# Kernel optimization log

Measured on AMD Instinct MI355X. Metric: run time of the kernel, lower is better.

Reference implementation:

```python
import jax, jax.numpy as jnp
import numpy as np


def setup_inputs() -> dict:
    key = jax.random.key(0)
    k1, k2, k3 = jax.random.split(key, 3)
    N, Ci, H, W = 16, 64, 224, 224
    Co, K = 128, 3
    x = jax.random.normal(k1, (N, Ci, H, W), dtype=jnp.float32)
    # Kaiming-like scale for conv weight
    conv_weight = jax.random.normal(k2, (Co, Ci, K, K), dtype=jnp.float32) * (1.0 / np.sqrt(Ci * K * K))
    conv_bias = jax.random.normal(k3, (Co,), dtype=jnp.float32) * 0.01
    return {"x": x, "conv_weight": conv_weight, "conv_bias": conv_bias}


def reference(x, conv_weight, conv_bias):
    # conv2d, stride=1, padding=0 (VALID), NCHW / OIHW
    y = jax.lax.conv_general_dilated(
        x, conv_weight,
        window_strides=(1, 1),
        padding="VALID",
        dimension_numbers=("NCHW", "OIHW", "NCHW"),
    ) + conv_bias[None, :, None, None]  # [N, Co, OH, OW]
    # min over output channels (keepdim), then double tanh
    m = jnp.min(y, axis=1, keepdims=True)  # [N, 1, OH, OW]
    return jnp.tanh(jnp.tanh(m))
```

## Files before the change

### kernel.cpp

```cpp
#include <hip/hip_runtime.h>
#include <hip/hip_bf16.h>
#include <math.h>

#define NN   16
#define CI   64
#define HH   224
#define WW   224
#define CO   128
#define OHH  222
#define OWW  222

#define WS_NEED (36*4*64*16)

typedef short  short8  __attribute__((ext_vector_type(8)));
typedef float  f32x16  __attribute__((ext_vector_type(16)));
typedef float  f32x4   __attribute__((ext_vector_type(4)));

__device__ static inline unsigned f2bf_pk(float a, float b) {
  __hip_bfloat162 h = __float22bfloat162_rn(make_float2(a, b));
  return *reinterpret_cast<unsigned*>(&h);
}

__global__ __launch_bounds__(256) void prep_w_kernel(const float* __restrict__ wt,
                                                     unsigned char* __restrict__ ws) {
  int t    = blockIdx.x * 256 + threadIdx.x;
  int lane = t & 63;
  int f    = t >> 6;
  int s    = f >> 2;
  int ct   = f & 3;
  int tap  = s >> 2;
  int cic  = s & 3;
  int kh   = tap / 3, kw = tap % 3;
  int co   = ct * 32 + (lane & 31);
  int k0   = cic * 16 + (lane >> 5) * 8;
  unsigned pk[4];
#pragma unroll
  for (int j = 0; j < 4; ++j) {
    int ci0 = k0 + 2 * j;
    float a = wt[(size_t)co * 576 + (ci0    ) * 9 + kh * 3 + kw];
    float b = wt[(size_t)co * 576 + (ci0 + 1) * 9 + kh * 3 + kw];
    pk[j] = f2bf_pk(a, b);
  }
  ((uint4*)ws)[t] = make_uint4(pk[0], pk[1], pk[2], pk[3]);
}

__global__ __launch_bounds__(512, 4) void conv_min_kernel(
    const float* __restrict__ x, const float* __restrict__ bias,
    const unsigned char* __restrict__ ws, float* __restrict__ out) {
  __shared__ __align__(16) unsigned char smem[6 * 34 * 128];

  int bid = blockIdx.x;
  bid = (bid & 7) * (NN * 56 * 7 / 8) + (bid >> 3);

  int owt  = bid % 7;
  int rest = bid / 7;
  int oht  = rest % 56;
  int n    = rest / 56;
  int ow0  = (owt < 6) ? owt * 32 : 190;
  int oh0  = oht * 4;

  int tid   = threadIdx.x;
  int wv    = tid >> 6;
  int lane  = tid & 63;
  int mg    = wv >> 1;
  int ng    = wv & 1;
  int mrow  = lane & 31;
  int khalf = lane >> 5;

  const short8* wf = (const short8*)ws;
  int bbase = ng * 128 + lane;
  short8 bb[3][2];
#pragma unroll
  for (int ct = 0; ct < 2; ++ct) bb[0][ct] = wf[0 * 256 + ct * 64 + bbase];
#pragma unroll
  for (int ct = 0; ct < 2; ++ct) bb[1][ct] = wf[1 * 256 + ct * 64 + bbase];

  {
    const float* xb = x + (size_t)n * 64 * 50176;
    int colm = (tid & 15) * 2;
    int q    = tid >> 4;
    int cc   = q >> 2, jw = (q & 3) * 4;
    int w0off = (((cc + colm    ) & 7) << 4) + jw;
    int w1off = (((cc + colm + 1) & 7) << 4) + jw;
    const float* xm = xb + (size_t)(q * 2) * 50176 + ow0 + colm;
    float2 A2[6], B2[6];
#pragma unroll
    for (int r = 0; r < 6; ++r) {
      int rg = oh0 + r; if (rg > 223) rg = 223;
      const float* s0 = xm + (size_t)rg * 224;
      A2[r] = *(const float2*)s0;
      B2[r] = *(const float2*)(s0 + 50176);
    }
    int re   = tid >> 6;
    int cole = 32 + ((tid >> 5) & 1);
    int ppe  = tid & 31;
    float ea = 0.f, eb = 0.f;
    const float* xe = xb + (size_t)(ppe * 2) * 50176 + ow0 + cole;
    if (re < 6) {
      int rg = oh0 + re; if (rg > 223) rg = 223;
      ea = xe[(size_t)rg * 224];
      eb = xe[(size_t)rg * 224 + 50176];
    }
#pragma unroll
    for (int r = 0; r < 6; ++r) {
      unsigned u0 = f2bf_pk(A2[r].x, B2[r].x);
      unsigned u1 = f2bf_pk(A2[r].y, B2[r].y);
      *(unsigned*)(smem + (r * 34 + colm    ) * 128 + w0off) = u0;
      *(unsigned*)(smem + (r * 34 + colm + 1) * 128 + w1off) = u1;
    }
    if (re < 6) {
      int eoff = ((((ppe >> 2) + cole) & 7) << 4) + (ppe & 3) * 4;
      *(unsigned*)(smem + (re * 34 + cole) * 128 + eoff) = f2bf_pk(ea, eb);
    }
  }

  f32x16 acc[2];
#pragma unroll
  for (int ct = 0; ct < 2; ++ct) {
    float bv = bias[ng * 64 + ct * 32 + mrow];
#pragma unroll
    for (int r = 0; r < 16; ++r) acc[ct][r] = bv;
  }

  unsigned uu = (mrow + khalf) & 7;
  const unsigned char* Pb = smem + (mg * 34 + mrow) * 128;
  const unsigned char* P[8];
#pragma unroll
  for (int j = 0; j < 8; ++j) P[j] = Pb + ((uu + j) & 7) * 16;

  __syncthreads();

  short8 aa[3];
  aa[0] = *(const short8*)(P[0]);
  aa[1] = *(const short8*)(P[2]);

#pragma unroll
  for (int s = 0; s < 36; ++s) {
    if (s + 2 < 36) {
#pragma unroll
      for (int ct = 0; ct < 2; ++ct)
        bb[(s + 2) % 3][ct] = wf[(s + 2) * 256 + ct * 64 + bbase];
      const int s2 = s + 2;
      const int kh2 = s2 / 12, kw2 = (s2 / 4) % 3, cic2 = s2 & 3;
      const int j2 = (2 * cic2 + kw2) & 7;
      aa[s2 % 3] = *(const short8*)(P[j2] + ((kh2 * 34 + kw2) << 7));
    }
#pragma unroll
    for (int ct = 0; ct < 2; ++ct)
      acc[ct] = __builtin_amdgcn_mfma_f32_32x32x16_bf16(
          aa[s % 3], bb[s % 3][ct], acc[ct], 0, 0, 0);
  }

  __syncthreads();
  float* epi = (float*)smem;
#pragma unroll
  for (int r = 0; r < 16; ++r) {
    float v = fminf(acc[0][r], acc[1][r]);
    v = fminf(v, __shfl_xor(v, 16, 64));
    if ((lane & 16) == 0) {
      int px = mg * 32 + ((r & 3) + 8 * (r >> 2) + 4 * khalf);
      epi[px * 36 + ng * 16 + (lane & 15)] = v;
    }
  }
  __syncthreads();
  if (tid < 128) {
    int px = tid;
    int oh = oh0 + (px >> 5);
    const f32x4* rowp = (const f32x4*)(epi + px * 36);
    f32x4 m4 = rowp[0];
#pragma unroll
    for (int k = 1; k < 8; ++k) {
      f32x4 t = rowp[k];
      m4[0] = fminf(m4[0], t[0]); m4[1] = fminf(m4[1], t[1]);
      m4[2] = fminf(m4[2], t[2]); m4[3] = fminf(m4[3], t[3]);
    }
    float v = fminf(fminf(m4[0], m4[1]), fminf(m4[2], m4[3]));
    v = tanhf(tanhf(v));
    if (oh < OHH)
      out[(size_t)n * (OHH * OWW) + (size_t)oh * OWW + ow0 + (px & 31)] = v;
  }
}

__global__ __launch_bounds__(128) void fallback_kernel(
    const float* __restrict__ x, const float* __restrict__ wt,
    const float* __restrict__ bias, float* __restrict__ out) {
  __shared__ float patch[64 * 30];
  __shared__ float red[128];
  int pb   = blockIdx.x;
  int owt  = pb % 28;
  int rest = pb / 28;
  int oh   = rest % OHH;
  int n    = rest / OHH;
  int ow0  = owt * 8;
  int tid  = threadIdx.x;
  for (int i = tid; i < 1920; i += 128) {
    int wl = i % 10;
    int rr = (i / 10) % 3;
    int ci = i / 30;
    int wg = ow0 + wl;
    float v = 0.f;
    if (wg < WW) v = x[((size_t)(n * 64 + ci) * HH + (oh + rr)) * WW + wg];
    patch[i] = v;
  }
  __syncthreads();
  int co = tid;
  float a[8];
#pragma unroll
  for (int p = 0; p < 8; ++p) a[p] = bias[co];
  for (int ci = 0; ci < 64; ++ci) {
#pragma unroll
    for (int rr = 0; rr < 3; ++rr)
#pragma unroll
      for (int kw = 0; kw < 3; ++kw) {
        float wvv = wt[(size_t)co * 576 + ci * 9 + rr * 3 + kw];
        const float* pp = &patch[ci * 30 + rr * 10 + kw];
#pragma unroll
        for (int p = 0; p < 8; ++p) a[p] += pp[p] * wvv;
      }
  }
  for (int p = 0; p < 8; ++p) {
    red[tid] = a[p];
    __syncthreads();
    for (int st = 64; st > 0; st >>= 1) {
      if (tid < st) red[tid] = fminf(red[tid], red[tid + st]);
      __syncthreads();
    }
    if (tid == 0 && (ow0 + p) < OWW)
      out[(size_t)n * (OHH * OWW) + (size_t)oh * OWW + ow0 + p] = tanhf(tanhf(red[0]));
    __syncthreads();
  }
}

extern "C" void kernel_launch(void* const* d_in, const int* in_sizes, int n_in,
                              void* d_out, int out_size, void* d_ws, size_t ws_size,
                              hipStream_t stream) {
  const float* x    = (const float*)d_in[0];
  const float* wt   = (const float*)d_in[1];
  const float* bias = (const float*)d_in[2];
  float* out        = (float*)d_out;

  if (ws_size >= WS_NEED) {
    unsigned char* ws = (unsigned char*)d_ws;
    prep_w_kernel<<<36, 256, 0, stream>>>(wt, ws);
    conv_min_kernel<<<NN * 56 * 7, 512, 0, stream>>>(x, bias, ws, out);
  } else {
    fallback_kernel<<<NN * OHH * 28, 128, 0, stream>>>(x, wt, bias, out);
  }
}
```

Before: 401.6 us.

## Stage conv weights through double-buffered LDS chunks instead of per-wave global loads

Weight fragments were read from global memory per wave (each of the 8 waves loading its own B fragments). Now the block cooperatively loads 24KB chunks of prepacked weights into a double-buffered LDS region, with a register-staged prefetch of the next chunk and a barrier per chunk. This cuts redundant global/L2 traffic for weights across the 4 mg waves but raises LDS use from ~26KB to ~75KB and adds 5 barriers, which may limit occupancy (launch_bounds requests 4 blocks).

```diff
diff --git a/kernel.cpp b/kernel.cpp
--- a/kernel.cpp
+++ b/kernel.cpp
@@ -11,6 +11,9 @@
 #define OWW  222
 
 #define WS_NEED (36*4*64*16)
+
+#define A_BYTES (6*34*128)
+#define BCHUNK  24576
 
 typedef short  short8  __attribute__((ext_vector_type(8)));
 typedef float  f32x16  __attribute__((ext_vector_type(16)));
@@ -47,7 +50,7 @@
 __global__ __launch_bounds__(512, 4) void conv_min_kernel(
     const float* __restrict__ x, const float* __restrict__ bias,
     const unsigned char* __restrict__ ws, float* __restrict__ out) {
-  __shared__ __align__(16) unsigned char smem[6 * 34 * 128];
+  __shared__ __align__(16) unsigned char smem[A_BYTES + 2 * BCHUNK];
 
   int bid = blockIdx.x;
   bid = (bid & 7) * (NN * 56 * 7 / 8) + (bid >> 3);
@@ -66,14 +69,6 @@
   int ng    = wv & 1;
   int mrow  = lane & 31;
   int khalf = lane >> 5;
-
-  const short8* wf = (const short8*)ws;
-  int bbase = ng * 128 + lane;
-  short8 bb[3][2];
-#pragma unroll
-  for (int ct = 0; ct < 2; ++ct) bb[0][ct] = wf[0 * 256 + ct * 64 + bbase];
-#pragma unroll
-  for (int ct = 0; ct < 2; ++ct) bb[1][ct] = wf[1 * 256 + ct * 64 + bbase];
 
   {
     const float* xb = x + (size_t)n * 64 * 50176;
@@ -91,6 +86,10 @@
       A2[r] = *(const float2*)s0;
       B2[r] = *(const float2*)(s0 + 50176);
     }
+    uint4 b0[3];
+#pragma unroll
+    for (int r = 0; r < 3; ++r)
+      b0[r] = *(const uint4*)(ws + r * 8192 + (size_t)tid * 16);
     int re   = tid >> 6;
     int cole = 32 + ((tid >> 5) & 1);
     int ppe  = tid & 31;
@@ -108,6 +107,9 @@
       *(unsigned*)(smem + (r * 34 + colm    ) * 128 + w0off) = u0;
       *(unsigned*)(smem + (r * 34 + colm + 1) * 128 + w1off) = u1;
     }
+#pragma unroll
+    for (int r = 0; r < 3; ++r)
+      *(uint4*)(smem + A_BYTES + r * 8192 + (size_t)tid * 16) = b0[r];
     if (re < 6) {
       int eoff = ((((ppe >> 2) + cole) & 7) << 4) + (ppe & 3) * 4;
       *(unsigned*)(smem + (re * 34 + cole) * 128 + eoff) = f2bf_pk(ea, eb);
@@ -128,27 +130,62 @@
 #pragma unroll
   for (int j = 0; j < 8; ++j) P[j] = Pb + ((uu + j) & 7) * 16;
 
+  const unsigned char* Bw = smem + A_BYTES + ng * 2048 + lane * 16;
+
   __syncthreads();
 
   short8 aa[3];
   aa[0] = *(const short8*)(P[0]);
   aa[1] = *(const short8*)(P[2]);
 
-#pragma unroll
-  for (int s = 0; s < 36; ++s) {
-    if (s + 2 < 36) {
+  short8 bb[3][2];
+#pragma unroll
+  for (int ct = 0; ct < 2; ++ct) {
+    bb[0][ct] = *(const short8*)(Bw + 0 * 4096 + ct * 1024);
+    bb[1][ct] = *(const short8*)(Bw + 1 * 4096 + ct * 1024);
+  }
+
+  uint4 breg[3];
+#pragma unroll
+  for (int ch = 0; ch < 6; ++ch) {
+    const int p = ch & 1;
+    if (ch + 1 < 6) {
+#pragma unroll
+      for (int r = 0; r < 3; ++r)
+        breg[r] = *(const uint4*)(ws + (ch + 1) * BCHUNK + r * 8192 + (size_t)tid * 16);
+    }
+#pragma unroll
+    for (int si = 0; si < 6; ++si) {
+      const int s = ch * 6 + si;
+      if (si + 2 < 6) {
+#pragma unroll
+        for (int ct = 0; ct < 2; ++ct)
+          bb[(si + 2) % 3][ct] =
+              *(const short8*)(Bw + p * BCHUNK + (si + 2) * 4096 + ct * 1024);
+      }
+      if (s + 2 < 36) {
+        const int s2 = s + 2;
+        const int kh2 = s2 / 12, kw2 = (s2 / 4) % 3, cic2 = s2 & 3;
+        const int j2 = (2 * cic2 + kw2) & 7;
+        aa[s2 % 3] = *(const short8*)(P[j2] + ((kh2 * 34 + kw2) << 7));
+      }
 #pragma unroll
       for (int ct = 0; ct < 2; ++ct)
-        bb[(s + 2) % 3][ct] = wf[(s + 2) * 256 + ct * 64 + bbase];
-      const int s2 = s + 2;
-      const int kh2 = s2 / 12, kw2 = (s2 / 4) % 3, cic2 = s2 & 3;
-      const int j2 = (2 * cic2 + kw2) & 7;
-      aa[s2 % 3] = *(const short8*)(P[j2] + ((kh2 * 34 + kw2) << 7));
-    }
-#pragma unroll
-    for (int ct = 0; ct < 2; ++ct)
-      acc[ct] = __builtin_amdgcn_mfma_f32_32x32x16_bf16(
-          aa[s % 3], bb[s % 3][ct], acc[ct], 0, 0, 0);
+        acc[ct] = __builtin_amdgcn_mfma_f32_32x32x16_bf16(
+            aa[s % 3], bb[si % 3][ct], acc[ct], 0, 0, 0);
+    }
+    if (ch + 1 < 6) {
+      unsigned char* dst = smem + A_BYTES + (p ^ 1) * BCHUNK + (size_t)tid * 16;
+#pragma unroll
+      for (int r = 0; r < 3; ++r)
+        *(uint4*)(dst + r * 8192) = breg[r];
+      __syncthreads();
+#pragma unroll
+      for (int ct = 0; ct < 2; ++ct) {
+        bb[0][ct] = *(const short8*)(Bw + (p ^ 1) * BCHUNK + 0 * 4096 + ct * 1024);
+        bb[1][ct] = *(const short8*)(Bw + (p ^ 1) * BCHUNK + 1 * 4096 + ct * 1024);
+      }
+    }
   }
 
   __syncthreads();
```

Result: faster. 372.9 us (-7.2%).
